# Kernel tuning notes

Measured on AMD Instinct MI355X. Metric: run time of the kernel, lower is better.

The kernel has to match this reference:

```python
import jax, jax.numpy as jnp
import numpy as np

B, S, F, RANK = 8, 4096, 1024, 64


def gram_schmidt(P):
    """Sequential Gram-Schmidt on columns of P (F, R) -> orthogonal (unnormalized) columns.
    Matches vizbert's orth_tensor: v_i = p_i - sum_{j<i} ((u_j . v)/(u_j . u_j)) u_j.
    Each step vectorizes the inner projection loop as one matmul (u_j are mutually
    orthogonal, so sequential-update and batched coefficients are equal in exact math)."""
    us = [P[:, 0]]
    for i in range(1, P.shape[1]):
        U = jnp.stack(us, axis=1)                 # (F, i)
        sq = jnp.sum(U * U, axis=0)               # (i,)
        v = P[:, i]
        coeff = (U.T @ v) / sq                    # (i,)
        us.append(v - U @ coeff)
    return jnp.stack(us, axis=1)                  # (F, R)


def setup_inputs() -> dict:
    key = jax.random.key(0)
    k1, k2 = jax.random.split(key)
    hidden_states = jax.random.normal(k1, (B, S, F), dtype=jnp.float32)
    # probe params initialized uniform(-0.05, 0.05), stacked to (num_features, rank)
    probe = jax.random.uniform(k2, (F, RANK), minval=-0.05, maxval=0.05, dtype=jnp.float32)
    return {"hidden_states": hidden_states, "probe": probe}


def reference(hidden_states, probe):
    # orth_probe: Gram-Schmidt orthogonalized probe columns (orthogonalize=True)
    U = gram_schmidt(probe)                       # (F, R), orthogonal columns
    sq = jnp.sum(U * U, axis=0)                   # (R,) squared norms

    # normalize=True: remember per-token norms before projection
    old_norms = jnp.linalg.norm(hidden_states, axis=2, keepdims=True)  # (B, S, 1)
    # mask_first=True: remember first-token states
    first_state = hidden_states[:, 0]             # (B, F)

    # full_batch_gs: subtract projection onto each probe direction.
    # Because U's columns are orthogonal, the sequential per-column subtraction
    # equals one fused projection: h - U (U^T h / ||u||^2).
    coeffs = jnp.einsum('bsf,fr->bsr', hidden_states, U) / sq
    h = hidden_states - jnp.einsum('bsr,fr->bsf', coeffs, U)

    # normalize=True: rescale back to the original per-token norm
    new_norms = jnp.linalg.norm(h, axis=2, keepdims=True)
    h = h / new_norms * old_norms

    # mask_first=True: restore the first token untouched
    h = h.at[:, 0].set(first_state)
    return h
```

## Files before the change

kernel.cpp:

```cpp
#include <hip/hip_runtime.h>


typedef __attribute__((ext_vector_type(8))) short bf16x8;
typedef __attribute__((ext_vector_type(4))) float f32x4;

#define MFMA_B16(a, b, c) __builtin_amdgcn_mfma_f32_16x16x32_bf16((a), (b), (c), 0, 0, 0)

__device__ __forceinline__ unsigned short bf16bits(float x) {
  union { float f; unsigned u; } v; v.f = x;
  return (unsigned short)((v.u + 0x7fffu + ((v.u >> 16) & 1u)) >> 16);
}

__global__ void pp_gram(const float* __restrict__ P, float* __restrict__ partial,
                        unsigned short* __restrict__ Ptf, unsigned short* __restrict__ Pbf) {
  __shared__ float Pl[64][68];
  const int tid = threadIdx.x, b = blockIdx.x;
  #pragma unroll
  for (int u = 0; u < 4; ++u) {
    const int f = tid >> 2, r = (tid & 3) * 16 + 4 * u;
    *(f32x4*)&Pl[f][r] = *(const f32x4*)(P + (size_t)(b * 64 + f) * 64 + r);
  }
  __syncthreads();

  #pragma unroll
  for (int u = 0; u < 2; ++u) {
    const int flat = tid + 256 * u;
    const int lf = flat >> 6, lane = flat & 63;
    const int c16 = lane & 15, quad = lane >> 4;
    const int it_loc = lf >> 2, t = lf & 3;
    const int flb = it_loc * 32 + quad * 8;
    bf16x8 w;
    #pragma unroll
    for (int e = 0; e < 8; ++e) w[e] = (short)bf16bits(Pl[flb + e][t * 16 + c16]);
    const int gidx = ((b >> 1) * 4 + 2 * (b & 1) + it_loc) * 4 + t;
    *(bf16x8*)(Ptf + ((size_t)gidx * 64 + lane) * 8) = w;
  }
  #pragma unroll
  for (int u = 0; u < 2; ++u) {
    const int flat = tid + 256 * u;
    const int lf = flat >> 6, lane = flat & 63;
    const int c16 = lane & 15, quad = lane >> 4;
    const int t2 = lf >> 1, j = lf & 1;
    f32x4 p0 = *(const f32x4*)&Pl[t2 * 16 + c16][j * 32 + quad * 8];
    f32x4 p1 = *(const f32x4*)&Pl[t2 * 16 + c16][j * 32 + quad * 8 + 4];
    bf16x8 w;
    #pragma unroll
    for (int e = 0; e < 4; ++e) { w[e] = (short)bf16bits(p0[e]); w[4 + e] = (short)bf16bits(p1[e]); }
    const int gidx = 2 * (b * 4 + t2) + j;
    *(bf16x8*)(Pbf + ((size_t)gidx * 64 + lane) * 8) = w;
  }

  const int a0 = (tid >> 4) * 4, b0 = (tid & 15) * 4;
  f32x4 acc[4];
  #pragma unroll
  for (int i = 0; i < 4; ++i) acc[i] = (f32x4){0.f, 0.f, 0.f, 0.f};
  for (int k = 0; k < 64; ++k) {
    f32x4 av = *(const f32x4*)&Pl[k][a0];
    f32x4 bv = *(const f32x4*)&Pl[k][b0];
    #pragma unroll
    for (int i = 0; i < 4; ++i) acc[i] += av[i] * bv;
  }
  #pragma unroll
  for (int i = 0; i < 4; ++i)
    *(f32x4*)(partial + (size_t)b * 4096 + (size_t)(a0 + i) * 64 + b0) = acc[i];
}

__global__ void pp_invert(const float* __restrict__ partial, unsigned short* __restrict__ Wf) {
  __shared__ float A[64][68];
  const int tid = threadIdx.x;
  const int i = tid >> 2, q16 = (tid & 3) * 16;
  #pragma unroll
  for (int u = 0; u < 4; ++u) {
    f32x4 s = (f32x4){0.f, 0.f, 0.f, 0.f};
    const int off = i * 64 + q16 + 4 * u;
    for (int p = 0; p < 16; ++p) s += *(const f32x4*)(partial + (size_t)p * 4096 + off);
    *(f32x4*)&A[i][q16 + 4 * u] = s;
  }
  __syncthreads();
  for (int k = 0; k < 64; ++k) {
    const float d = 1.0f / A[k][k];
    const float f = A[i][k];
    f32x4 prs[4], cur[4];
    #pragma unroll
    for (int u = 0; u < 4; ++u) {
      prs[u] = *(const f32x4*)&A[k][q16 + 4 * u];
      cur[u] = *(const f32x4*)&A[i][q16 + 4 * u];
    }
    __syncthreads();
    const int kl = k - q16;
    #pragma unroll
    for (int u = 0; u < 4; ++u) {
      f32x4 pv = prs[u] * d;
      if (kl >= u * 4 && kl < u * 4 + 4) { pv[kl - u * 4] = d; cur[u][kl - u * 4] = 0.f; }
      f32x4 res = (i == k) ? pv : (cur[u] - f * pv);
      *(f32x4*)&A[i][q16 + 4 * u] = res;
    }
    __syncthreads();
  }
  #pragma unroll
  for (int u = 0; u < 2; ++u) {
    const int flat = tid + 256 * u;
    const int lf = flat >> 6, lane = flat & 63;
    const int c16 = lane & 15, quad = lane >> 4;
    const int kk = lf >> 2, tf = lf & 3;
    bf16x8 w;
    #pragma unroll
    for (int e = 0; e < 8; ++e) w[e] = (short)bf16bits(A[kk * 32 + quad * 8 + e][tf * 16 + c16]);
    *(bf16x8*)(Wf + ((size_t)(kk * 4 + tf) * 64 + lane) * 8) = w;
  }
}

__device__ __forceinline__ void ld_chunk(const float* __restrict__ hp, int ch, f32x4* v) {
  #pragma unroll
  for (int it = 0; it < 4; ++it) {
    v[2 * it] = *(const f32x4*)(hp + ch * 128 + it * 32);
    v[2 * it + 1] = *(const f32x4*)(hp + ch * 128 + it * 32 + 4);
  }
}

__device__ __forceinline__ void comp_chunk(const f32x4* v, const unsigned short* __restrict__ bp0,
                                           int ch, f32x4* accY, float& sqacc) {
  #pragma unroll
  for (int it = 0; it < 4; ++it) {
    const f32x4 v0 = v[2 * it], v1 = v[2 * it + 1];
    sqacc += v0[0] * v0[0] + v0[1] * v0[1] + v0[2] * v0[2] + v0[3] * v0[3] +
             v1[0] * v1[0] + v1[1] * v1[1] + v1[2] * v1[2] + v1[3] * v1[3];
    bf16x8 a;
    a[0] = (short)bf16bits(v0[0]); a[1] = (short)bf16bits(v0[1]);
    a[2] = (short)bf16bits(v0[2]); a[3] = (short)bf16bits(v0[3]);
    a[4] = (short)bf16bits(v1[0]); a[5] = (short)bf16bits(v1[1]);
    a[6] = (short)bf16bits(v1[2]); a[7] = (short)bf16bits(v1[3]);
    #pragma unroll
    for (int t = 0; t < 4; ++t) {
      bf16x8 b = *(const bf16x8*)(bp0 + (size_t)((ch * 4 + it) * 4 + t) * 512);
      accY[t] = MFMA_B16(a, b, accY[t]);
    }
  }
}

__global__ __launch_bounds__(256, 2) void pp_y(
    const float* __restrict__ H, const unsigned short* __restrict__ Ptf,
    const unsigned short* __restrict__ Wf, unsigned short* __restrict__ Cf,
    float* __restrict__ Sc) {
  __shared__ __align__(16) unsigned short Yt[4][16][72];
  __shared__ __align__(16) unsigned short Ct[4][16][72];

  const int tid = threadIdx.x;
  const int lane = tid & 63, wid = tid >> 6;
  const int c16 = lane & 15, quad = lane >> 4;
  const int strip = wid * 16;
  const long row0 = (long)blockIdx.x * 64;

  f32x4 accY[4];
  #pragma unroll
  for (int t = 0; t < 4; ++t) accY[t] = (f32x4){0.f, 0.f, 0.f, 0.f};
  float sqacc = 0.f;
  const float* hp = H + (row0 + strip + c16) * 1024 + quad * 8;
  const unsigned short* bp0 = Ptf + lane * 8;

  {
    f32x4 va[8], vb[8];
    ld_chunk(hp, 0, va);
    ld_chunk(hp, 1, vb);
    comp_chunk(va, bp0, 0, accY, sqacc); ld_chunk(hp, 2, va);
    comp_chunk(vb, bp0, 1, accY, sqacc); ld_chunk(hp, 3, vb);
    comp_chunk(va, bp0, 2, accY, sqacc); ld_chunk(hp, 4, va);
    comp_chunk(vb, bp0, 3, accY, sqacc); ld_chunk(hp, 5, vb);
    comp_chunk(va, bp0, 4, accY, sqacc); ld_chunk(hp, 6, va);
    comp_chunk(vb, bp0, 5, accY, sqacc); ld_chunk(hp, 7, vb);
    comp_chunk(va, bp0, 6, accY, sqacc);
    comp_chunk(vb, bp0, 7, accY, sqacc);
  }

  sqacc += __shfl_xor(sqacc, 16);
  sqacc += __shfl_xor(sqacc, 32);

  #pragma unroll
  for (int t = 0; t < 4; ++t)
    #pragma unroll
    for (int r = 0; r < 4; ++r)
      Yt[wid][quad * 4 + r][t * 16 + c16] = bf16bits(accY[t][r]);

  f32x4 accC[4];
  #pragma unroll
  for (int t = 0; t < 4; ++t) accC[t] = (f32x4){0.f, 0.f, 0.f, 0.f};
  #pragma unroll
  for (int kk = 0; kk < 2; ++kk) {
    bf16x8 a = *(const bf16x8*)&Yt[wid][c16][kk * 32 + quad * 8];
    #pragma unroll
    for (int t = 0; t < 4; ++t) {
      bf16x8 b = *(const bf16x8*)(Wf + ((size_t)(kk * 4 + t) * 64 + lane) * 8);
      accC[t] = MFMA_B16(a, b, accC[t]);
    }
  }
  #pragma unroll
  for (int t = 0; t < 4; ++t)
    #pragma unroll
    for (int r = 0; r < 4; ++r)
      Ct[wid][quad * 4 + r][t * 16 + c16] = bf16bits(accC[t][r]);

  #pragma unroll
  for (int r = 0; r < 4; ++r) {
    float dd = accY[0][r] * accC[0][r] + accY[1][r] * accC[1][r] +
               accY[2][r] * accC[2][r] + accY[3][r] * accC[3][r];
    dd += __shfl_xor(dd, 1);
    dd += __shfl_xor(dd, 2);
    dd += __shfl_xor(dd, 4);
    dd += __shfl_xor(dd, 8);
    const float o2 = __shfl(sqacc, quad * 4 + r);
    if (c16 == 0) {
      const float n2 = fmaxf(o2 - dd, 1e-30f);
      Sc[row0 + strip + quad * 4 + r] = sqrtf(o2 / n2);
    }
  }

  bf16x8 cb0 = *(const bf16x8*)&Ct[wid][c16][quad * 8];
  bf16x8 cb1 = *(const bf16x8*)&Ct[wid][c16][32 + quad * 8];
  const size_t s = (size_t)(row0 + strip) >> 4;
  *(bf16x8*)(Cf + (s * 2 + 0) * 512 + lane * 8) = cb0;
  *(bf16x8*)(Cf + (s * 2 + 1) * 512 + lane * 8) = cb1;
}

__global__ __launch_bounds__(256, 2) void pp_apply(
    const float* __restrict__ H, const unsigned short* __restrict__ Pbf,
    const unsigned short* __restrict__ Cf, const float* __restrict__ Sc,
    float* __restrict__ out) {
  const int tid = threadIdx.x;
  const int lane = tid & 63, wid = tid >> 6;
  const int c16 = lane & 15, quad = lane >> 4;
  const int strip = wid * 16;
  const long row0 = (long)blockIdx.x * 64;

  const size_t s = (size_t)(row0 + strip) >> 4;
  const bf16x8 cb0 = *(const bf16x8*)(Cf + (s * 2 + 0) * 512 + lane * 8);
  const bf16x8 cb1 = *(const bf16x8*)(Cf + (s * 2 + 1) * 512 + lane * 8);

  const long grow = row0 + strip + c16;
  const float sc = Sc[grow];
  const bool fs = ((grow & 4095) == 0);
  const float* hp = H + grow * 1024 + quad * 4;
  float* op = out + grow * 1024 + quad * 4;
  const unsigned short* pb = Pbf + lane * 8;

  f32x4 hbuf[4];
  bf16x8 abuf[2][2];
  #pragma unroll
  for (int i = 0; i < 4; ++i) hbuf[i] = *(const f32x4*)(hp + (size_t)i * 16);
  #pragma unroll
  for (int i = 0; i < 2; ++i) {
    abuf[i][0] = *(const bf16x8*)(pb + (size_t)(2 * i + 0) * 512);
    abuf[i][1] = *(const bf16x8*)(pb + (size_t)(2 * i + 1) * 512);
  }

  #pragma unroll 4
  for (int ft = 0; ft < 64; ++ft) {
    const f32x4 hcur = hbuf[ft & 3];
    const bf16x8 pa0 = abuf[ft & 1][0];
    const bf16x8 pa1 = abuf[ft & 1][1];
    if (ft + 4 < 64) hbuf[ft & 3] = *(const f32x4*)(hp + (size_t)(ft + 4) * 16);
    if (ft + 2 < 64) {
      abuf[ft & 1][0] = *(const bf16x8*)(pb + (size_t)(2 * (ft + 2) + 0) * 512);
      abuf[ft & 1][1] = *(const bf16x8*)(pb + (size_t)(2 * (ft + 2) + 1) * 512);
    }
    f32x4 acc = (f32x4){0.f, 0.f, 0.f, 0.f};
    acc = MFMA_B16(pa0, cb0, acc);
    acc = MFMA_B16(pa1, cb1, acc);
    f32x4 o;
    #pragma unroll
    for (int e = 0; e < 4; ++e) o[e] = (hcur[e] - acc[e]) * sc;
    if (fs) o = hcur;
    *(f32x4*)(op + (size_t)ft * 16) = o;
  }
}

extern "C" void kernel_launch(void* const* d_in, const int* in_sizes, int n_in,
                              void* d_out, int out_size, void* d_ws, size_t ws_size,
                              hipStream_t stream) {
  const float* H = (const float*)d_in[0];
  const float* P = (const float*)d_in[1];
  float* out = (float*)d_out;
  float* partial = (float*)d_ws;
  unsigned short* Ptf = (unsigned short*)(partial + 16 * 4096);
  unsigned short* Pbf = Ptf + 65536;
  unsigned short* Wf = Pbf + 65536;
  float* Sc = (float*)(Wf + 4096);
  unsigned short* Cf = (unsigned short*)(Sc + 32768);

  pp_gram<<<16, 256, 0, stream>>>(P, partial, Ptf, Pbf);
  pp_invert<<<1, 256, 0, stream>>>(partial, Wf);
  pp_y<<<512, 256, 0, stream>>>(H, Ptf, Wf, Cf, Sc);
  pp_apply<<<512, 256, 0, stream>>>(H, Pbf, Cf, Sc, out);
}
```

Baseline: 329.5 us.

## Fuse invert, projection and apply kernels with flag-synchronized producer block

Merges the Gram-inverse kernel, the coefficient kernel and the apply kernel into one launch. Block 0 computes the inverse and publishes it through a global release flag, and the other blocks acquire-wait on that flag after their first projection pass. Coefficients and scales stay in shared memory instead of going through a global round trip. The intent is to remove two launches and the Cf/Sc traffic and to overlap the inversion with streaming H. The cost is a spin-wait that assumes block 0 gets scheduled, an extra memset, and a second read of H that now happens inside the same block.

```diff
diff --git a/kernel.cpp b/kernel.cpp
--- a/kernel.cpp
+++ b/kernel.cpp
@@ -63,51 +63,6 @@
   #pragma unroll
   for (int i = 0; i < 4; ++i)
     *(f32x4*)(partial + (size_t)b * 4096 + (size_t)(a0 + i) * 64 + b0) = acc[i];
-}
-
-__global__ void pp_invert(const float* __restrict__ partial, unsigned short* __restrict__ Wf) {
-  __shared__ float A[64][68];
-  const int tid = threadIdx.x;
-  const int i = tid >> 2, q16 = (tid & 3) * 16;
-  #pragma unroll
-  for (int u = 0; u < 4; ++u) {
-    f32x4 s = (f32x4){0.f, 0.f, 0.f, 0.f};
-    const int off = i * 64 + q16 + 4 * u;
-    for (int p = 0; p < 16; ++p) s += *(const f32x4*)(partial + (size_t)p * 4096 + off);
-    *(f32x4*)&A[i][q16 + 4 * u] = s;
-  }
-  __syncthreads();
-  for (int k = 0; k < 64; ++k) {
-    const float d = 1.0f / A[k][k];
-    const float f = A[i][k];
-    f32x4 prs[4], cur[4];
-    #pragma unroll
-    for (int u = 0; u < 4; ++u) {
-      prs[u] = *(const f32x4*)&A[k][q16 + 4 * u];
-      cur[u] = *(const f32x4*)&A[i][q16 + 4 * u];
-    }
-    __syncthreads();
-    const int kl = k - q16;
-    #pragma unroll
-    for (int u = 0; u < 4; ++u) {
-      f32x4 pv = prs[u] * d;
-      if (kl >= u * 4 && kl < u * 4 + 4) { pv[kl - u * 4] = d; cur[u][kl - u * 4] = 0.f; }
-      f32x4 res = (i == k) ? pv : (cur[u] - f * pv);
-      *(f32x4*)&A[i][q16 + 4 * u] = res;
-    }
-    __syncthreads();
-  }
-  #pragma unroll
-  for (int u = 0; u < 2; ++u) {
-    const int flat = tid + 256 * u;
-    const int lf = flat >> 6, lane = flat & 63;
-    const int c16 = lane & 15, quad = lane >> 4;
-    const int kk = lf >> 2, tf = lf & 3;
-    bf16x8 w;
-    #pragma unroll
-    for (int e = 0; e < 8; ++e) w[e] = (short)bf16bits(A[kk * 32 + quad * 8 + e][tf * 16 + c16]);
-    *(bf16x8*)(Wf + ((size_t)(kk * 4 + tf) * 64 + lane) * 8) = w;
-  }
 }
 
 __device__ __forceinline__ void ld_chunk(const float* __restrict__ hp, int ch, f32x4* v) {
@@ -138,18 +93,71 @@
   }
 }
 
-__global__ __launch_bounds__(256, 2) void pp_y(
-    const float* __restrict__ H, const unsigned short* __restrict__ Ptf,
-    const unsigned short* __restrict__ Wf, unsigned short* __restrict__ Cf,
-    float* __restrict__ Sc) {
-  __shared__ __align__(16) unsigned short Yt[4][16][72];
-  __shared__ __align__(16) unsigned short Ct[4][16][72];
-
+__global__ __launch_bounds__(256, 3) void pp_fused(
+    const float* __restrict__ H, const float* __restrict__ partial,
+    const unsigned short* __restrict__ Ptf, const unsigned short* __restrict__ Pbf,
+    unsigned short* __restrict__ Wf, unsigned int* __restrict__ flag,
+    float* __restrict__ out) {
+  __shared__ __align__(16) unsigned char smem[18688];
   const int tid = threadIdx.x;
   const int lane = tid & 63, wid = tid >> 6;
   const int c16 = lane & 15, quad = lane >> 4;
+
+  if (blockIdx.x == 0) {
+    float (*A)[68] = (float(*)[68])smem;
+    const int i = tid >> 2, q16 = (tid & 3) * 16;
+    #pragma unroll
+    for (int u = 0; u < 4; ++u) {
+      f32x4 s = (f32x4){0.f, 0.f, 0.f, 0.f};
+      const int off = i * 64 + q16 + 4 * u;
+      for (int p = 0; p < 16; ++p) s += *(const f32x4*)(partial + (size_t)p * 4096 + off);
+      *(f32x4*)&A[i][q16 + 4 * u] = s;
+    }
+    __syncthreads();
+    for (int k = 0; k < 64; ++k) {
+      const float d = 1.0f / A[k][k];
+      const float f = A[i][k];
+      f32x4 prs[4], cur[4];
+      #pragma unroll
+      for (int u = 0; u < 4; ++u) {
+        prs[u] = *(const f32x4*)&A[k][q16 + 4 * u];
+        cur[u] = *(const f32x4*)&A[i][q16 + 4 * u];
+      }
+      __syncthreads();
+      const int kl = k - q16;
+      #pragma unroll
+      for (int u = 0; u < 4; ++u) {
+        f32x4 pv = prs[u] * d;
+        if (kl >= u * 4 && kl < u * 4 + 4) { pv[kl - u * 4] = d; cur[u][kl - u * 4] = 0.f; }
+        f32x4 res = (i == k) ? pv : (cur[u] - f * pv);
+        *(f32x4*)&A[i][q16 + 4 * u] = res;
+      }
+      __syncthreads();
+    }
+    #pragma unroll
+    for (int u = 0; u < 2; ++u) {
+      const int flat = tid + 256 * u;
+      const int lf = flat >> 6, ln = flat & 63;
+      const int lc = ln & 15, lq = ln >> 4;
+      const int kk = lf >> 2, tf = lf & 3;
+      bf16x8 w;
+      #pragma unroll
+      for (int e = 0; e < 8; ++e) w[e] = (short)bf16bits(A[kk * 32 + lq * 8 + e][tf * 16 + lc]);
+      *(bf16x8*)(Wf + ((size_t)(kk * 4 + tf) * 64 + ln) * 8) = w;
+    }
+    __threadfence();
+    __syncthreads();
+    if (tid == 0)
+      __hip_atomic_store(flag, 1u, __ATOMIC_RELEASE, __HIP_MEMORY_SCOPE_AGENT);
+    return;
+  }
+
+  unsigned short (*Yt)[72] = (unsigned short(*)[72])smem;
+  unsigned short (*Ct)[72] = (unsigned short(*)[72])(smem + 9216);
+  float* scT = (float*)(smem + 18432);
+  const int wb = blockIdx.x - 1;
   const int strip = wid * 16;
-  const long row0 = (long)blockIdx.x * 64;
+  const long row0 = (long)wb * 64;
 
   f32x4 accY[4];
   #pragma unroll
@@ -157,7 +165,6 @@
   float sqacc = 0.f;
   const float* hp = H + (row0 + strip + c16) * 1024 + quad * 8;
   const unsigned short* bp0 = Ptf + lane * 8;
-
   {
     f32x4 va[8], vb[8];
     ld_chunk(hp, 0, va);
@@ -179,14 +186,21 @@
   for (int t = 0; t < 4; ++t)
     #pragma unroll
     for (int r = 0; r < 4; ++r)
-      Yt[wid][quad * 4 + r][t * 16 + c16] = bf16bits(accY[t][r]);
+      Yt[strip + quad * 4 + r][t * 16 + c16] = bf16bits(accY[t][r]);
+
+  if (tid == 0) {
+    while (__hip_atomic_load(flag, __ATOMIC_ACQUIRE, __HIP_MEMORY_SCOPE_AGENT) == 0u)
+      __builtin_amdgcn_s_sleep(2);
+  }
+  __syncthreads();
+  __threadfence();
 
   f32x4 accC[4];
   #pragma unroll
   for (int t = 0; t < 4; ++t) accC[t] = (f32x4){0.f, 0.f, 0.f, 0.f};
   #pragma unroll
   for (int kk = 0; kk < 2; ++kk) {
-    bf16x8 a = *(const bf16x8*)&Yt[wid][c16][kk * 32 + quad * 8];
+    bf16x8 a = *(const bf16x8*)&Yt[strip + c16][kk * 32 + quad * 8];
     #pragma unroll
     for (int t = 0; t < 4; ++t) {
       bf16x8 b = *(const bf16x8*)(Wf + ((size_t)(kk * 4 + t) * 64 + lane) * 8);
@@ -197,7 +211,7 @@
   for (int t = 0; t < 4; ++t)
     #pragma unroll
     for (int r = 0; r < 4; ++r)
-      Ct[wid][quad * 4 + r][t * 16 + c16] = bf16bits(accC[t][r]);
+      Ct[strip + quad * 4 + r][t * 16 + c16] = bf16bits(accC[t][r]);
 
   #pragma unroll
   for (int r = 0; r < 4; ++r) {
@@ -210,46 +224,27 @@
     const float o2 = __shfl(sqacc, quad * 4 + r);
     if (c16 == 0) {
       const float n2 = fmaxf(o2 - dd, 1e-30f);
-      Sc[row0 + strip + quad * 4 + r] = sqrtf(o2 / n2);
-    }
-  }
-
-  bf16x8 cb0 = *(const bf16x8*)&Ct[wid][c16][quad * 8];
-  bf16x8 cb1 = *(const bf16x8*)&Ct[wid][c16][32 + quad * 8];
-  const size_t s = (size_t)(row0 + strip) >> 4;
-  *(bf16x8*)(Cf + (s * 2 + 0) * 512 + lane * 8) = cb0;
-  *(bf16x8*)(Cf + (s * 2 + 1) * 512 + lane * 8) = cb1;
-}
-
-__global__ __launch_bounds__(256, 2) void pp_apply(
-    const float* __restrict__ H, const unsigned short* __restrict__ Pbf,
-    const unsigned short* __restrict__ Cf, const float* __restrict__ Sc,
-    float* __restrict__ out) {
-  const int tid = threadIdx.x;
-  const int lane = tid & 63, wid = tid >> 6;
-  const int c16 = lane & 15, quad = lane >> 4;
-  const int strip = wid * 16;
-  const long row0 = (long)blockIdx.x * 64;
-
-  const size_t s = (size_t)(row0 + strip) >> 4;
-  const bf16x8 cb0 = *(const bf16x8*)(Cf + (s * 2 + 0) * 512 + lane * 8);
-  const bf16x8 cb1 = *(const bf16x8*)(Cf + (s * 2 + 1) * 512 + lane * 8);
-
+      scT[strip + quad * 4 + r] = sqrtf(o2 / n2);
+    }
+  }
+
+  bf16x8 cb0 = *(const bf16x8*)&Ct[strip + c16][quad * 8];
+  bf16x8 cb1 = *(const bf16x8*)&Ct[strip + c16][32 + quad * 8];
   const long grow = row0 + strip + c16;
-  const float sc = Sc[grow];
+  const float sc = scT[strip + c16];
   const bool fs = ((grow & 4095) == 0);
-  const float* hp = H + grow * 1024 + quad * 4;
+  const float* hp2 = H + grow * 1024 + quad * 4;
   float* op = out + grow * 1024 + quad * 4;
   const unsigned short* pb = Pbf + lane * 8;
 
   f32x4 hbuf[4];
   bf16x8 abuf[2][2];
   #pragma unroll
-  for (int i = 0; i < 4; ++i) hbuf[i] = *(const f32x4*)(hp + (size_t)i * 16);
-  #pragma unroll
-  for (int i = 0; i < 2; ++i) {
-    abuf[i][0] = *(const bf16x8*)(pb + (size_t)(2 * i + 0) * 512);
-    abuf[i][1] = *(const bf16x8*)(pb + (size_t)(2 * i + 1) * 512);
+  for (int i2 = 0; i2 < 4; ++i2) hbuf[i2] = *(const f32x4*)(hp2 + (size_t)i2 * 16);
+  #pragma unroll
+  for (int i2 = 0; i2 < 2; ++i2) {
+    abuf[i2][0] = *(const bf16x8*)(pb + (size_t)(2 * i2 + 0) * 512);
+    abuf[i2][1] = *(const bf16x8*)(pb + (size_t)(2 * i2 + 1) * 512);
   }
 
   #pragma unroll 4
@@ -257,7 +252,7 @@
     const f32x4 hcur = hbuf[ft & 3];
     const bf16x8 pa0 = abuf[ft & 1][0];
     const bf16x8 pa1 = abuf[ft & 1][1];
-    if (ft + 4 < 64) hbuf[ft & 3] = *(const f32x4*)(hp + (size_t)(ft + 4) * 16);
+    if (ft + 4 < 64) hbuf[ft & 3] = *(const f32x4*)(hp2 + (size_t)(ft + 4) * 16);
     if (ft + 2 < 64) {
       abuf[ft & 1][0] = *(const bf16x8*)(pb + (size_t)(2 * (ft + 2) + 0) * 512);
       abuf[ft & 1][1] = *(const bf16x8*)(pb + (size_t)(2 * (ft + 2) + 1) * 512);
@@ -283,11 +278,9 @@
   unsigned short* Ptf = (unsigned short*)(partial + 16 * 4096);
   unsigned short* Pbf = Ptf + 65536;
   unsigned short* Wf = Pbf + 65536;
-  float* Sc = (float*)(Wf + 4096);
-  unsigned short* Cf = (unsigned short*)(Sc + 32768);
-
+  unsigned int* flag = (unsigned int*)(Wf + 4096);
+
+  hipMemsetAsync(flag, 0, sizeof(unsigned int), stream);
   pp_gram<<<16, 256, 0, stream>>>(P, partial, Ptf, Pbf);
-  pp_invert<<<1, 256, 0, stream>>>(partial, Wf);
-  pp_y<<<512, 256, 0, stream>>>(H, Ptf, Wf, Cf, Sc);
-  pp_apply<<<512, 256, 0, stream>>>(H, Pbf, Cf, Sc, out);
-}
+  pp_fused<<<513, 256, 0, stream>>>(H, partial, Ptf, Pbf, Wf, flag, out);
+}
```

New measurement: 361.0 us. 9.6% more time.
